# Kernel tuning notes

Hardware: AMD Instinct MI355X
Metric: run time of the kernel (lower is better)

Reference implementation:

```python
import jax, jax.numpy as jnp
import numpy as np
import math

B, DIM, N, H, G, NK = 256, 384, 128, 4, 2, 4
DH = DIM // H   # 96 head dim
DG = DIM // G   # 192 per offset group
KS = 7          # offset depthwise kernel
DFF = 2048
OFFSET_SCALE = 4.0
EPS = 1e-5

def _ln(x, g, b):
    m = jnp.mean(x, -1, keepdims=True)
    v = jnp.mean((x - m) ** 2, -1, keepdims=True)
    return (x - m) * jax.lax.rsqrt(v + EPS) * g + b

def _mlp2(x, W1, b1, W2, b2):
    return jax.nn.relu(x @ W1 + b1) @ W2 + b2

def _forward(q_raw, kv_raw, emb_q, ln_pq_g, ln_pq_b, emb_kv, ln_pkv_g, ln_pkv_b,
             Wq1, bq1, Wq2, bq2, Wk1, bk1, Wk2, bk2, Wv1, bv1, Wv2, bv2,
             dw_w, dw_b, pw_w, ln1_g, ln1_b, ln2_g, ln2_b, Wf1, bf1, Wf2, bf2, attn_scale):
    # learned positional encodings (Embedding + LayerNorm), added on channel-first layout
    q_raw = q_raw + _ln(emb_q[:N], ln_pq_g, ln_pq_b).T[None]           # (B, DIM, N)
    kv_raw = kv_raw + _ln(emb_kv[:N], ln_pkv_g, ln_pkv_b).T[None]
    # query projection: Linear-ReLU-Linear over channel dim (dropout = identity, eval)
    q = _mlp2(q_raw.transpose(0, 2, 1), Wq1, bq1, Wq2, bq2).transpose(0, 2, 1)  # (B, DIM, N)
    # offset prediction: depthwise conv -> GELU -> 1x1 conv -> tanh * scale
    gq = q.reshape(B * G, DG, N)
    pad = (KS - 1) // 2
    off = jax.lax.conv_general_dilated(gq, dw_w, (1,), [(pad, pad)],
                                       dimension_numbers=('NCH', 'OIH', 'NCH'),
                                       feature_group_count=DG) + dw_b[None, :, None]
    off = jax.nn.gelu(off, approximate=False)
    off = jnp.einsum('bcn,kc->bkn', off, pw_w)
    off = jnp.tanh(off) * OFFSET_SCALE                                 # (B*G, NK, N)
    vgrid = jnp.arange(N, dtype=off.dtype) + off
    vg = jnp.clip(2.0 * vgrid / (N - 1) - 1.0, -1.0, 1.0)              # (B*G, NK, N)
    # 1D bilinear grid_sample, zero padding, align_corners=False
    gkv = kv_raw.reshape(B * G, DG, N)
    iy = ((vg.reshape(B * G, NK * N) + 1.0) * N - 1.0) / 2.0           # unnormalized coord
    y0 = jnp.floor(iy)
    w = (iy - y0)[:, None, :]
    y0i = y0.astype(jnp.int32)
    def samp(yi):
        valid = ((yi >= 0) & (yi < N)).astype(gkv.dtype)[:, None, :]
        idx = jnp.broadcast_to(jnp.clip(yi, 0, N - 1)[:, None, :], (B * G, DG, NK * N))
        return jnp.take_along_axis(gkv, idx, axis=2) * valid
    sampled = samp(y0i) * (1.0 - w) + samp(y0i + 1) * w                # (B*G, DG, NK*N)
    # '(b g) num_k d n -> (b num_k) (g d) n'
    kv_feats = sampled.reshape(B, G, DG, NK, N).transpose(0, 3, 1, 2, 4).reshape(B * NK, DIM, N)
    k = _mlp2(kv_feats.transpose(0, 2, 1), Wk1, bk1, Wk2, bk2)         # (B*NK, N, DIM)
    v = _mlp2(kv_feats.transpose(0, 2, 1), Wv1, bv1, Wv2, bv2)
    # per-position attention: each query attends over its NK sampled kv
    qh = (q * DH ** -0.5).reshape(B, H, DH, N).transpose(0, 3, 1, 2)   # (B, N, H, DH)
    def heads(t):  # (B*NK, N, DIM) -> (B, N, H, NK, DH)
        return t.reshape(B, NK, N, H, DH).transpose(0, 2, 3, 1, 4)
    kh, vh = heads(k), heads(v)
    # NB: original code's `headdim = q.size(-1)` picks up the seq dim (N), kept faithfully
    sim = jnp.einsum('bnhd,bnhjd->bnhj', qh, kh) / math.sqrt(N)
    sim = sim - jax.lax.stop_gradient(jnp.max(sim, -1, keepdims=True))
    attn = jax.nn.softmax(sim * attn_scale, axis=-1)
    out = jnp.einsum('bnhj,bnhjd->bnhd', attn, vh).reshape(B, N, DIM)
    res = _ln(q_raw.transpose(0, 2, 1) + out, ln1_g, ln1_b)
    res = res + _mlp2(res, Wf1, bf1, Wf2, bf2)
    return _ln(res, ln2_g, ln2_b).transpose(0, 2, 1)                   # (B, DIM, N)

def setup_inputs() -> dict:
    key = jax.random.key(0)
    ks = iter(jax.random.split(key, 24))
    def nrm(shape, s=0.05):
        return jax.random.normal(next(ks), shape, dtype=jnp.float32) * s
    return dict(
        q_raw=jax.random.normal(next(ks), (B, DIM, N), dtype=jnp.float32),
        kv_raw=jax.random.normal(next(ks), (B, DIM, N), dtype=jnp.float32),
        emb_q=nrm((128, DIM), 1.0), ln_pq_g=jnp.ones((DIM,), jnp.float32), ln_pq_b=jnp.zeros((DIM,), jnp.float32),
        emb_kv=nrm((128, DIM), 1.0), ln_pkv_g=jnp.ones((DIM,), jnp.float32), ln_pkv_b=jnp.zeros((DIM,), jnp.float32),
        Wq1=nrm((DIM, DIM)), bq1=jnp.zeros((DIM,), jnp.float32), Wq2=nrm((DIM, DIM)), bq2=jnp.zeros((DIM,), jnp.float32),
        Wk1=nrm((DIM, DIM)), bk1=jnp.zeros((DIM,), jnp.float32), Wk2=nrm((DIM, DIM)), bk2=jnp.zeros((DIM,), jnp.float32),
        Wv1=nrm((DIM, DIM)), bv1=jnp.zeros((DIM,), jnp.float32), Wv2=nrm((DIM, DIM)), bv2=jnp.zeros((DIM,), jnp.float32),
        dw_w=nrm((DG, 1, KS)), dw_b=jnp.zeros((DG,), jnp.float32), pw_w=nrm((NK, DG)),
        ln1_g=jnp.ones((DIM,), jnp.float32), ln1_b=jnp.zeros((DIM,), jnp.float32),
        ln2_g=jnp.ones((DIM,), jnp.float32), ln2_b=jnp.zeros((DIM,), jnp.float32),
        Wf1=nrm((DIM, DFF)), bf1=jnp.zeros((DFF,), jnp.float32), Wf2=nrm((DFF, DIM)), bf2=jnp.zeros((DIM,), jnp.float32),
        attn_scale=jnp.asarray(70.0, jnp.float32),
    )

def reference(q_raw, kv_raw, emb_q, ln_pq_g, ln_pq_b, emb_kv, ln_pkv_g, ln_pkv_b,
              Wq1, bq1, Wq2, bq2, Wk1, bk1, Wk2, bk2, Wv1, bv1, Wv2, bv2,
              dw_w, dw_b, pw_w, ln1_g, ln1_b, ln2_g, ln2_b, Wf1, bf1, Wf2, bf2, attn_scale):
    return _forward(q_raw, kv_raw, emb_q, ln_pq_g, ln_pq_b, emb_kv, ln_pkv_g, ln_pkv_b,
                    Wq1, bq1, Wq2, bq2, Wk1, bk1, Wk2, bk2, Wv1, bv1, Wv2, bv2,
                    dw_w, dw_b, pw_w, ln1_g, ln1_b, ln2_g, ln2_b, Wf1, bf1, Wf2, bf2, attn_scale)
```

## Files before the change

### kernel.cpp

```cpp
#include <hip/hip_runtime.h>
#include <hip/hip_bf16.h>
#include <cstdint>
#include <cstddef>

#define BB   256
#define DIM  384
#define NN   128
#define NH   4
#define NG   2
#define NKK  4
#define DHH  96
#define DG   192
#define KSZ  7
#define DFF  2048

typedef __attribute__((ext_vector_type(8))) short bf8_t;
typedef __attribute__((ext_vector_type(4))) float f4_t;

static __device__ __forceinline__ float geluf(float x) {
  return 0.5f * x * (1.0f + erff(x * 0.70710678118654752440f));
}
static __device__ __forceinline__ short f2bf(float f) {
  union { __hip_bfloat16 h; short s; } u;
  u.h = __float2bfloat16(f);
  return u.s;
}

template<bool WB>
__global__ __launch_bounds__(128) void ln_rows_kernel(
    const float* __restrict__ X,
    const float* __restrict__ gam, const float* __restrict__ bet,
    float* __restrict__ out, __hip_bfloat16* __restrict__ out2)
{
  const int row = blockIdx.x;
  const int t = threadIdx.x;
  const size_t base = (size_t)row * DIM;
  float x0 = X[base + t], x1 = X[base + t + 128], x2 = X[base + t + 256];
  __shared__ float ws[2];
  float s = x0 + x1 + x2;
#pragma unroll
  for (int o = 32; o; o >>= 1) s += __shfl_down(s, o);
  if ((t & 63) == 0) ws[t >> 6] = s;
  __syncthreads();
  const float m = (ws[0] + ws[1]) * (1.0f / DIM);
  __syncthreads();
  const float d0 = x0 - m, d1 = x1 - m, d2 = x2 - m;
  float v = d0 * d0 + d1 * d1 + d2 * d2;
#pragma unroll
  for (int o = 32; o; o >>= 1) v += __shfl_down(v, o);
  if ((t & 63) == 0) ws[t >> 6] = v;
  __syncthreads();
  const float var = (ws[0] + ws[1]) * (1.0f / DIM);
  const float rs = rsqrtf(var + 1e-5f);
  const float o0 = d0 * rs * gam[t]       + bet[t];
  const float o1 = d1 * rs * gam[t + 128] + bet[t + 128];
  const float o2 = d2 * rs * gam[t + 256] + bet[t + 256];
  out[base + t] = o0; out[base + t + 128] = o1; out[base + t + 256] = o2;
  if (WB) {
    out2[base + t]       = __float2bfloat16(o0);
    out2[base + t + 128] = __float2bfloat16(o1);
    out2[base + t + 256] = __float2bfloat16(o2);
  }
}

template<bool WB>
__global__ __launch_bounds__(256) void transpose_addpe(
    const float* __restrict__ X, const float* __restrict__ pe,
    float* __restrict__ out, __hip_bfloat16* __restrict__ outb)
{
  __shared__ float tile[32][33];
  const int b = blockIdx.z;
  const int n0 = blockIdx.x * 32, d0 = blockIdx.y * 32;
  const int tx = threadIdx.x, ty = threadIdx.y;
#pragma unroll
  for (int i = 0; i < 4; i++) {
    const int d = d0 + ty + i * 8;
    tile[ty + i * 8][tx] = X[(size_t)b * DIM * NN + (size_t)d * NN + n0 + tx];
  }
  __syncthreads();
#pragma unroll
  for (int i = 0; i < 4; i++) {
    const int n = n0 + ty + i * 8;
    const int d = d0 + tx;
    const float v = tile[tx][ty + i * 8] + pe[n * DIM + d];
    out[((size_t)b * NN + n) * DIM + d] = v;
    if (WB) outb[((size_t)b * NN + n) * DIM + d] = __float2bfloat16(v);
  }
}

__global__ __launch_bounds__(256) void transpose_to_cf(
    const float* __restrict__ rows, float* __restrict__ out)
{
  __shared__ float tile[32][33];
  const int b = blockIdx.z;
  const int n0 = blockIdx.x * 32, d0 = blockIdx.y * 32;
  const int tx = threadIdx.x, ty = threadIdx.y;
#pragma unroll
  for (int i = 0; i < 4; i++) {
    const int n = n0 + ty + i * 8;
    tile[ty + i * 8][tx] = rows[((size_t)b * NN + n) * DIM + d0 + tx];
  }
  __syncthreads();
#pragma unroll
  for (int i = 0; i < 4; i++) {
    const int d = d0 + ty + i * 8;
    out[(size_t)b * DIM * NN + (size_t)d * NN + n0 + tx] = tile[tx][ty + i * 8];
  }
}

__global__ __launch_bounds__(256) void wtrans_kernel(
    const float* __restrict__ W, __hip_bfloat16* __restrict__ WT, int K, int N)
{
  __shared__ float tile[32][33];
  const int n0 = blockIdx.x * 32, k0 = blockIdx.y * 32;
  const int tx = threadIdx.x, ty = threadIdx.y;
#pragma unroll
  for (int i = 0; i < 4; i++)
    tile[ty + i * 8][tx] = W[(size_t)(k0 + ty + i * 8) * N + n0 + tx];
  __syncthreads();
#pragma unroll
  for (int i = 0; i < 4; i++)
    WT[(size_t)(n0 + ty + i * 8) * K + k0 + tx] =
        __float2bfloat16(tile[tx][ty + i * 8]);
}

#define LDP 40
template<bool RELU, bool RES, bool OUTBF>
__global__ __launch_bounds__(256) void mfma_gemm_kernel(
    const __hip_bfloat16* __restrict__ A, const __hip_bfloat16* __restrict__ BT,
    const float* __restrict__ bias, const float* __restrict__ resid,
    float* __restrict__ outf, __hip_bfloat16* __restrict__ outb,
    int K, int Nc, int lda)
{
  __shared__ __align__(16) short As[128 * LDP];
  __shared__ __align__(16) short Bs[128 * LDP];
  const int tid = threadIdx.x;
  const int lane = tid & 63, wid = tid >> 6;
  const int wm = wid >> 1, wn = wid & 1;
  const size_t rowBase = (size_t)blockIdx.y * 128;
  const size_t colBase = (size_t)blockIdx.x * 128;
  f4_t acc[4][4] = {};
  const int lr = lane & 15, lg = lane >> 4;
  for (int k0 = 0; k0 < K; k0 += 32) {
#pragma unroll
    for (int l = 0; l < 2; l++) {
      const int c = tid + l * 256;
      const int r = c >> 2, ko = (c & 3) * 8;
      *(uint4*)&As[r * LDP + ko] =
          *(const uint4*)&A[(rowBase + r) * (size_t)lda + k0 + ko];
      *(uint4*)&Bs[r * LDP + ko] =
          *(const uint4*)&BT[(colBase + r) * (size_t)K + k0 + ko];
    }
    __syncthreads();
    bf8_t af[4], bfr[4];
#pragma unroll
    for (int mi = 0; mi < 4; mi++)
      af[mi] = *(const bf8_t*)&As[(wm * 64 + mi * 16 + lr) * LDP + lg * 8];
#pragma unroll
    for (int ni = 0; ni < 4; ni++)
      bfr[ni] = *(const bf8_t*)&Bs[(wn * 64 + ni * 16 + lr) * LDP + lg * 8];
#pragma unroll
    for (int mi = 0; mi < 4; mi++)
#pragma unroll
      for (int ni = 0; ni < 4; ni++)
        acc[mi][ni] = __builtin_amdgcn_mfma_f32_16x16x32_bf16(
            af[mi], bfr[ni], acc[mi][ni], 0, 0, 0);
    __syncthreads();
  }
#pragma unroll
  for (int ni = 0; ni < 4; ni++) {
    const size_t col = colBase + wn * 64 + ni * 16 + lr;
    const float bv = bias[col];
#pragma unroll
    for (int mi = 0; mi < 4; mi++) {
#pragma unroll
      for (int r = 0; r < 4; r++) {
        const size_t row = rowBase + wm * 64 + mi * 16 + lg * 4 + r;
        float v = acc[mi][ni][r] + bv;
        if (RELU) v = fmaxf(v, 0.0f);
        if (RES) v += resid[row * Nc + col];
        if (OUTBF) outb[row * Nc + col] = __float2bfloat16(v);
        else       outf[row * Nc + col] = v;
      }
    }
  }
}

__global__ __launch_bounds__(256) void mfma_gemm_sampled_kv(
    const float* __restrict__ kvrows, const int* __restrict__ y0buf,
    const float* __restrict__ wbuf, const __hip_bfloat16* __restrict__ BT,
    const float* __restrict__ biasK, const float* __restrict__ biasV,
    __hip_bfloat16* __restrict__ outb, int byBase)
{
  const int K = DIM, Nc = 2 * DIM;
  __shared__ __align__(16) short As[128 * LDP];
  __shared__ __align__(16) short Bs[128 * LDP];
  const int tid = threadIdx.x;
  const int lane = tid & 63, wid = tid >> 6;
  const int wm = wid >> 1, wn = wid & 1;
  const int byG = blockIdx.y + byBase;
  const int b = byG >> 2, kk = byG & 3;
  const size_t rowBase = (size_t)blockIdx.y * 128;
  const size_t colBase = (size_t)blockIdx.x * 128;
  f4_t acc[4][4] = {};
  const int lr = lane & 15, lg = lane >> 4;
  for (int k0 = 0; k0 < K; k0 += 32) {
#pragma unroll
    for (int l = 0; l < 2; l++) {
      const int c = tid + l * 256;
      const int r = c >> 2, ko = (c & 3) * 8;
      const int d = k0 + ko;
      const int g = d / DG;
      const int sidx = (((b * NG + g) * NKK) + kk) * NN + r;
      const int y0 = y0buf[sidx];
      const float w = wbuf[sidx];
      float4 a0 = make_float4(0.f, 0.f, 0.f, 0.f), a1 = a0, b0 = a0, b1 = a0;
      if (y0 >= 0) {
        const float* p = &kvrows[((size_t)b * NN + y0) * DIM + d];
        a0 = *(const float4*)p; a1 = *(const float4*)(p + 4);
      }
      if (y0 < NN - 1) {
        const float* p = &kvrows[((size_t)b * NN + y0 + 1) * DIM + d];
        b0 = *(const float4*)p; b1 = *(const float4*)(p + 4);
      }
      const float w0 = 1.0f - w;
      short sv[8];
      sv[0] = f2bf(a0.x * w0 + b0.x * w); sv[1] = f2bf(a0.y * w0 + b0.y * w);
      sv[2] = f2bf(a0.z * w0 + b0.z * w); sv[3] = f2bf(a0.w * w0 + b0.w * w);
      sv[4] = f2bf(a1.x * w0 + b1.x * w); sv[5] = f2bf(a1.y * w0 + b1.y * w);
      sv[6] = f2bf(a1.z * w0 + b1.z * w); sv[7] = f2bf(a1.w * w0 + b1.w * w);
      *(uint4*)&As[r * LDP + ko] = *(const uint4*)&sv[0];
      *(uint4*)&Bs[r * LDP + ko] =
          *(const uint4*)&BT[(colBase + r) * (size_t)K + k0 + ko];
    }
    __syncthreads();
    bf8_t af[4], bfr[4];
#pragma unroll
    for (int mi = 0; mi < 4; mi++)
      af[mi] = *(const bf8_t*)&As[(wm * 64 + mi * 16 + lr) * LDP + lg * 8];
#pragma unroll
    for (int ni = 0; ni < 4; ni++)
      bfr[ni] = *(const bf8_t*)&Bs[(wn * 64 + ni * 16 + lr) * LDP + lg * 8];
#pragma unroll
    for (int mi = 0; mi < 4; mi++)
#pragma unroll
      for (int ni = 0; ni < 4; ni++)
        acc[mi][ni] = __builtin_amdgcn_mfma_f32_16x16x32_bf16(
            af[mi], bfr[ni], acc[mi][ni], 0, 0, 0);
    __syncthreads();
  }
  const float* bp = (colBase < (size_t)DIM) ? biasK : biasV;
  const int cofs = (colBase < (size_t)DIM) ? 0 : DIM;
#pragma unroll
  for (int ni = 0; ni < 4; ni++) {
    const size_t col = colBase + wn * 64 + ni * 16 + lr;
    const float bv = bp[col - cofs];
#pragma unroll
    for (int mi = 0; mi < 4; mi++) {
#pragma unroll
      for (int r = 0; r < 4; r++) {
        const size_t row = rowBase + wm * 64 + mi * 16 + lg * 4 + r;
        const float v = fmaxf(acc[mi][ni][r] + bv, 0.0f);
        outb[row * Nc + col] = __float2bfloat16(v);
      }
    }
  }
}

__global__ __launch_bounds__(192) void offset3_kernel(
    const float* __restrict__ qproj, const float* __restrict__ dw_w,
    const float* __restrict__ dw_b, const float* __restrict__ pw_w,
    int* __restrict__ y0buf, float* __restrict__ wbuf)
{
  const int bg = blockIdx.x;
  const int n0 = blockIdx.y * 16;
  const int b = bg >> 1, g = bg & 1;
  const int t = threadIdx.x;
  const int lane = t & 63, wv = t >> 6;
  __shared__ float part[16][3][4];

  const float* qp = qproj + (size_t)b * NN * DIM + g * DG + t;
  float dwc[KSZ];
#pragma unroll
  for (int tap = 0; tap < KSZ; ++tap) dwc[tap] = dw_w[t * KSZ + tap];
  const float db = dw_b[t];
  const float pw0 = pw_w[0 * DG + t], pw1 = pw_w[1 * DG + t];
  const float pw2 = pw_w[2 * DG + t], pw3 = pw_w[3 * DG + t];

  float x[16 + KSZ - 1];
#pragma unroll
  for (int j = 0; j < 16 + KSZ - 1; ++j) {
    const int np = n0 - 3 + j;
    x[j] = ((unsigned)np < (unsigned)NN) ? qp[(size_t)np * DIM] : 0.f;
  }
#pragma unroll
  for (int j = 0; j < 16; ++j) {
    float y = db;
#pragma unroll
    for (int i = 0; i < KSZ; ++i) y = fmaf(x[j + i], dwc[i], y);
    const float gl = geluf(y);
    float p0 = pw0 * gl, p1 = pw1 * gl, p2 = pw2 * gl, p3 = pw3 * gl;
#pragma unroll
    for (int o = 32; o; o >>= 1) {
      p0 += __shfl_down(p0, o);
      p1 += __shfl_down(p1, o);
      p2 += __shfl_down(p2, o);
      p3 += __shfl_down(p3, o);
    }
    if (lane == 0) {
      part[j][wv][0] = p0; part[j][wv][1] = p1;
      part[j][wv][2] = p2; part[j][wv][3] = p3;
    }
  }
  __syncthreads();
  if (t < 64) {
    const int j = t >> 2, kk = t & 3;
    const int n = n0 + j;
    const float acc = part[j][0][kk] + part[j][1][kk] + part[j][2][kk];
    const float off = tanhf(acc) * 4.0f;
    const float vgrid = (float)n + off;
    float vg = 2.0f * vgrid / (float)(NN - 1) - 1.0f;
    vg = fminf(fmaxf(vg, -1.0f), 1.0f);
    const float iy = ((vg + 1.0f) * (float)NN - 1.0f) * 0.5f;
    const float y0f = floorf(iy);
    const int idx = (bg * NKK + kk) * NN + n;
    y0buf[idx] = (int)y0f;
    wbuf[idx] = iy - y0f;
  }
}

__global__ __launch_bounds__(128) void attn_kernel(
    const float* __restrict__ qproj, const float* __restrict__ k_ch,
    const float* __restrict__ v_ch, const float* __restrict__ attn_scale,
    float* __restrict__ qrows, int bBase)
{
  const int bid = blockIdx.x;
  const int h = bid & 3;
  const int bnl = bid >> 2;
  const int bl = bnl >> 7;
  const int n = bnl & 127;
  const size_t bn = ((size_t)(bBase + bl)) * NN + n;
  const int t = threadIdx.x;
  const int lane = t & 63, wid = t >> 6;
  __shared__ float red[2][4];
  __shared__ float simsh[4];
  float qv = 0.f;
  if (t < DHH)
    qv = qproj[bn * DIM + h * DHH + t] * 0.10206207261596577f;
#pragma unroll
  for (int kk = 0; kk < NKK; kk++) {
    float pv = 0.f;
    if (t < DHH)
      pv = qv * k_ch[(((size_t)bl * NKK + kk) * NN + n) * DIM + h * DHH + t];
#pragma unroll
    for (int o = 32; o; o >>= 1) pv += __shfl_down(pv, o);
    if (lane == 0) red[wid][kk] = pv;
  }
  __syncthreads();
  if (t == 0) {
#pragma unroll
    for (int kk = 0; kk < NKK; kk++)
      simsh[kk] = (red[0][kk] + red[1][kk]) * 0.08838834764831845f;
  }
  __syncthreads();
  const float s0 = simsh[0], s1 = simsh[1], s2 = simsh[2], s3 = simsh[3];
  const float m = fmaxf(fmaxf(s0, s1), fmaxf(s2, s3));
  const float sc = attn_scale[0];
  const float e0 = expf((s0 - m) * sc), e1 = expf((s1 - m) * sc);
  const float e2 = expf((s2 - m) * sc), e3 = expf((s3 - m) * sc);
  const float inv = 1.0f / (e0 + e1 + e2 + e3);
  if (t < DHH) {
    const size_t vb = ((size_t)bl * NKK * NN + n) * DIM + h * DHH + t;
    const size_t stride = (size_t)NN * DIM;
    float o = e0 * inv * v_ch[vb];
    o += e1 * inv * v_ch[vb + stride];
    o += e2 * inv * v_ch[vb + 2 * stride];
    o += e3 * inv * v_ch[vb + 3 * stride];
    const size_t oi = bn * DIM + h * DHH + t;
    qrows[oi] = qrows[oi] + o;
  }
}

extern "C" void kernel_launch(void* const* d_in, const int* in_sizes, int n_in,
                              void* d_out, int out_size, void* d_ws, size_t ws_size,
                              hipStream_t stream)
{
  const float* q_raw    = (const float*)d_in[0];
  const float* kv_raw   = (const float*)d_in[1];
  const float* emb_q    = (const float*)d_in[2];
  const float* ln_pq_g  = (const float*)d_in[3];
  const float* ln_pq_b  = (const float*)d_in[4];
  const float* emb_kv   = (const float*)d_in[5];
  const float* ln_pkv_g = (const float*)d_in[6];
  const float* ln_pkv_b = (const float*)d_in[7];
  const float* Wq1 = (const float*)d_in[8];   const float* bq1 = (const float*)d_in[9];
  const float* Wq2 = (const float*)d_in[10];  const float* bq2 = (const float*)d_in[11];
  const float* Wk1 = (const float*)d_in[12];  const float* bk1 = (const float*)d_in[13];
  const float* Wk2 = (const float*)d_in[14];  const float* bk2 = (const float*)d_in[15];
  const float* Wv1 = (const float*)d_in[16];  const float* bv1 = (const float*)d_in[17];
  const float* Wv2 = (const float*)d_in[18];  const float* bv2 = (const float*)d_in[19];
  const float* dw_w = (const float*)d_in[20]; const float* dw_b = (const float*)d_in[21];
  const float* pw_w = (const float*)d_in[22];
  const float* ln1_g = (const float*)d_in[23]; const float* ln1_b = (const float*)d_in[24];
  const float* ln2_g = (const float*)d_in[25]; const float* ln2_b = (const float*)d_in[26];
  const float* Wf1 = (const float*)d_in[27];  const float* bf1 = (const float*)d_in[28];
  const float* Wf2 = (const float*)d_in[29];  const float* bf2 = (const float*)d_in[30];
  const float* attn_scale = (const float*)d_in[31];
  float* out = (float*)d_out;

  const size_t S = (size_t)BB * NN * DIM;
  const size_t TAILF = 4 * 73728 + 147456 + 2 * 393216 + 2 * (size_t)NN * DIM
                     + 2 * (size_t)BB * NG * NKK * NN;
  int NCH = 16, NFQ = 8;
  {
    const int cand[5][2] = {{2, 1}, {4, 1}, {8, 2}, {16, 4}, {16, 8}};
    for (int i = 0; i < 5; i++) {
      const size_t rows = (size_t)(BB / cand[i][0]) * NKK * NN;
      size_t ch = S;
      const size_t pb = rows * 1152;
      const size_t pc = S / 2 + (size_t)33554432 / cand[i][1];
      if (pb > ch) ch = pb;
      if (pc > ch) ch = pc;
      const size_t totB = (3 * S + ch + TAILF) * 4;
      if (totB <= ws_size) { NCH = cand[i][0]; NFQ = cand[i][1]; break; }
    }
  }
  const int MQ = BB * NN;
  const int B_PER_CH = BB / NCH;
  const int BY_PER_CH = B_PER_CH * NKK;
  const int ROWS_PER_CH = BY_PER_CH * NN;
  const int FROWS = MQ / NFQ;
  size_t CHSZ = S;
  {
    const size_t pb = (size_t)ROWS_PER_CH * 1152;
    const size_t pc = S / 2 + (size_t)33554432 / NFQ;
    if (pb > CHSZ) CHSZ = pb;
    if (pc > CHSZ) CHSZ = pc;
  }

  float* wsf = (float*)d_ws;
  float* qrows = wsf;
  float* kvr   = qrows + S;
  float* qproj = kvr + S;
  float* chbase = qproj + S;
  __hip_bfloat16* qrows_bf = (__hip_bfloat16*)chbase;
  __hip_bfloat16* scr_bf   = (__hip_bfloat16*)(chbase + S / 2);
  __hip_bfloat16* hidkv_bf = (__hip_bfloat16*)chbase;
  float* k_ch = chbase + (size_t)ROWS_PER_CH * DIM;
  float* v_ch = k_ch + (size_t)ROWS_PER_CH * DIM;
  __hip_bfloat16* res_bf = (__hip_bfloat16*)chbase;
  __hip_bfloat16* ffnh   = (__hip_bfloat16*)(chbase + S / 2);
  float* p = chbase + CHSZ;
  __hip_bfloat16* wtq1  = (__hip_bfloat16*)p; p += 73728;
  __hip_bfloat16* wtq2  = (__hip_bfloat16*)p; p += 73728;
  __hip_bfloat16* wtkv1 = (__hip_bfloat16*)p; p += 147456;
  __hip_bfloat16* wtk2  = (__hip_bfloat16*)p; p += 73728;
  __hip_bfloat16* wtv2  = (__hip_bfloat16*)p; p += 73728;
  __hip_bfloat16* wtf1  = (__hip_bfloat16*)p; p += 393216;
  __hip_bfloat16* wtf2  = (__hip_bfloat16*)p; p += 393216;
  float* peq  = p; p += (size_t)NN * DIM;
  float* pekv = p; p += (size_t)NN * DIM;
  int*   y0buf = (int*)p; p += (size_t)BB * NG * NKK * NN;
  float* wbuf  = p;
  float* res   = kvr;
  float* res2  = qproj;
  float* lnout = qrows;

  wtrans_kernel<<<dim3(DIM/32, DIM/32), dim3(32, 8), 0, stream>>>(Wq1, wtq1, DIM, DIM);
  wtrans_kernel<<<dim3(DIM/32, DIM/32), dim3(32, 8), 0, stream>>>(Wq2, wtq2, DIM, DIM);
  wtrans_kernel<<<dim3(DIM/32, DIM/32), dim3(32, 8), 0, stream>>>(Wk1, wtkv1, DIM, DIM);
  wtrans_kernel<<<dim3(DIM/32, DIM/32), dim3(32, 8), 0, stream>>>(
      Wv1, wtkv1 + (size_t)DIM * DIM, DIM, DIM);
  wtrans_kernel<<<dim3(DIM/32, DIM/32), dim3(32, 8), 0, stream>>>(Wk2, wtk2, DIM, DIM);
  wtrans_kernel<<<dim3(DIM/32, DIM/32), dim3(32, 8), 0, stream>>>(Wv2, wtv2, DIM, DIM);
  wtrans_kernel<<<dim3(DFF/32, DIM/32), dim3(32, 8), 0, stream>>>(Wf1, wtf1, DIM, DFF);
  wtrans_kernel<<<dim3(DIM/32, DFF/32), dim3(32, 8), 0, stream>>>(Wf2, wtf2, DFF, DIM);

  ln_rows_kernel<false><<<dim3(NN), dim3(128), 0, stream>>>(
      emb_q, ln_pq_g, ln_pq_b, peq, nullptr);
  ln_rows_kernel<false><<<dim3(NN), dim3(128), 0, stream>>>(
      emb_kv, ln_pkv_g, ln_pkv_b, pekv, nullptr);

  transpose_addpe<true><<<dim3(NN/32, DIM/32, BB), dim3(32, 8), 0, stream>>>(
      q_raw, peq, qrows, qrows_bf);
  transpose_addpe<false><<<dim3(NN/32, DIM/32, BB), dim3(32, 8), 0, stream>>>(
      kv_raw, pekv, kvr, nullptr);

  mfma_gemm_kernel<true, false, true><<<dim3(DIM/128, MQ/128), 256, 0, stream>>>(
      qrows_bf, wtq1, bq1, nullptr, nullptr, scr_bf, DIM, DIM, DIM);
  mfma_gemm_kernel<false, false, false><<<dim3(DIM/128, MQ/128), 256, 0, stream>>>(
      scr_bf, wtq2, bq2, nullptr, qproj, nullptr, DIM, DIM, DIM);

  offset3_kernel<<<dim3(BB * NG, NN / 16), dim3(192), 0, stream>>>(
      qproj, dw_w, dw_b, pw_w, y0buf, wbuf);

  for (int c = 0; c < NCH; ++c) {
    const int byBase = c * BY_PER_CH;
    mfma_gemm_sampled_kv<<<dim3(2 * DIM / 128, BY_PER_CH), 256, 0, stream>>>(
        kvr, y0buf, wbuf, wtkv1, bk1, bv1, hidkv_bf, byBase);
    mfma_gemm_kernel<false, false, false><<<dim3(DIM/128, ROWS_PER_CH/128), 256, 0, stream>>>(
        hidkv_bf, wtk2, bk2, nullptr, k_ch, nullptr, DIM, DIM, 2 * DIM);
    mfma_gemm_kernel<false, false, false><<<dim3(DIM/128, ROWS_PER_CH/128), 256, 0, stream>>>(
        hidkv_bf + DIM, wtv2, bv2, nullptr, v_ch, nullptr, DIM, DIM, 2 * DIM);
    attn_kernel<<<dim3(B_PER_CH * NN * NH), 128, 0, stream>>>(
        qproj, k_ch, v_ch, attn_scale, qrows, c * B_PER_CH);
  }

  ln_rows_kernel<true><<<dim3(MQ), dim3(128), 0, stream>>>(
      qrows, ln1_g, ln1_b, res, res_bf);

  for (int q = 0; q < NFQ; ++q) {
    const size_t roff = (size_t)q * FROWS;
    mfma_gemm_kernel<true, false, true><<<dim3(DFF/128, FROWS/128), 256, 0, stream>>>(
        res_bf + roff * DIM, wtf1, bf1, nullptr, nullptr, ffnh, DIM, DFF, DIM);
    mfma_gemm_kernel<false, true, false><<<dim3(DIM/128, FROWS/128), 256, 0, stream>>>(
        ffnh, wtf2, bf2, res + roff * DIM, res2 + roff * DIM, nullptr, DFF, DIM, DFF);
  }

  ln_rows_kernel<false><<<dim3(MQ), dim3(128), 0, stream>>>(
      res2, ln2_g, ln2_b, lnout, nullptr);
  transpose_to_cf<<<dim3(NN/32, DIM/32, BB), dim3(32, 8), 0, stream>>>(
      lnout, out);
}
```

Measured before the change: 1.266 ms.

## Split bilinear sampling out of KV GEMM, merge K/V second GEMMs, add XCD swizzle

```diff
diff --git a/kernel.cpp b/kernel.cpp
--- a/kernel.cpp
+++ b/kernel.cpp
@@ -26,6 +26,18 @@
   return u.s;
 }
 
+static __device__ __forceinline__ void xcd_swizzle(int& bx, int& by) {
+  const int gx = gridDim.x;
+  const int nwg = gx * gridDim.y;
+  const int flat = by * gx + bx;
+  const int q = nwg >> 3, r = nwg & 7;
+  const int xcd = flat & 7, idx = flat >> 3;
+  const int logical =
+      (xcd < r ? xcd * (q + 1) : r * (q + 1) + (xcd - r) * q) + idx;
+  bx = logical % gx;
+  by = logical / gx;
+}
+
 template<bool WB>
 __global__ __launch_bounds__(128) void ln_rows_kernel(
     const float* __restrict__ X,
@@ -124,6 +136,14 @@
         __float2bfloat16(tile[tx][ty + i * 8]);
 }
 
+__global__ __launch_bounds__(256) void concat_bias_kernel(
+    const float* __restrict__ a, const float* __restrict__ b,
+    float* __restrict__ o, int n)
+{
+  const int i = blockIdx.x * 256 + threadIdx.x;
+  if (i < 2 * n) o[i] = (i < n) ? a[i] : b[i - n];
+}
+
 #define LDP 40
 template<bool RELU, bool RES, bool OUTBF>
 __global__ __launch_bounds__(256) void mfma_gemm_kernel(
@@ -137,8 +157,10 @@
   const int tid = threadIdx.x;
   const int lane = tid & 63, wid = tid >> 6;
   const int wm = wid >> 1, wn = wid & 1;
-  const size_t rowBase = (size_t)blockIdx.y * 128;
-  const size_t colBase = (size_t)blockIdx.x * 128;
+  int bx = blockIdx.x, by = blockIdx.y;
+  xcd_swizzle(bx, by);
+  const size_t rowBase = (size_t)by * 128;
+  const size_t colBase = (size_t)bx * 128;
   f4_t acc[4][4] = {};
   const int lr = lane & 15, lg = lane >> 4;
   for (int k0 = 0; k0 < K; k0 += 32) {
@@ -186,22 +208,29 @@
   }
 }
 
-__global__ __launch_bounds__(256) void mfma_gemm_sampled_kv(
-    const float* __restrict__ kvrows, const int* __restrict__ y0buf,
-    const float* __restrict__ wbuf, const __hip_bfloat16* __restrict__ BT,
+__global__ __launch_bounds__(256) void mfma_gemm_kv2(
+    const __hip_bfloat16* __restrict__ hidkv,
+    const __hip_bfloat16* __restrict__ BTk, const __hip_bfloat16* __restrict__ BTv,
     const float* __restrict__ biasK, const float* __restrict__ biasV,
-    __hip_bfloat16* __restrict__ outb, int byBase)
-{
-  const int K = DIM, Nc = 2 * DIM;
+    float* __restrict__ outK, float* __restrict__ outV)
+{
+  const int K = DIM, Nc = DIM, lda = 2 * DIM;
   __shared__ __align__(16) short As[128 * LDP];
   __shared__ __align__(16) short Bs[128 * LDP];
   const int tid = threadIdx.x;
   const int lane = tid & 63, wid = tid >> 6;
   const int wm = wid >> 1, wn = wid & 1;
-  const int byG = blockIdx.y + byBase;
-  const int b = byG >> 2, kk = byG & 3;
-  const size_t rowBase = (size_t)blockIdx.y * 128;
-  const size_t colBase = (size_t)blockIdx.x * 128;
+  int bx = blockIdx.x, by = blockIdx.y;
+  xcd_swizzle(bx, by);
+  const int nbyh = gridDim.y >> 1;
+  const int half = (by >= nbyh) ? 1 : 0;
+  const int byl = by - half * nbyh;
+  const __hip_bfloat16* A = hidkv + half * DIM;
+  const __hip_bfloat16* BT = half ? BTv : BTk;
+  const float* bias = half ? biasV : biasK;
+  float* outf = half ? outV : outK;
+  const size_t rowBase = (size_t)byl * 128;
+  const size_t colBase = (size_t)bx * 128;
   f4_t acc[4][4] = {};
   const int lr = lane & 15, lg = lane >> 4;
   for (int k0 = 0; k0 < K; k0 += 32) {
@@ -209,27 +238,8 @@
     for (int l = 0; l < 2; l++) {
       const int c = tid + l * 256;
       const int r = c >> 2, ko = (c & 3) * 8;
-      const int d = k0 + ko;
-      const int g = d / DG;
-      const int sidx = (((b * NG + g) * NKK) + kk) * NN + r;
-      const int y0 = y0buf[sidx];
-      const float w = wbuf[sidx];
-      float4 a0 = make_float4(0.f, 0.f, 0.f, 0.f), a1 = a0, b0 = a0, b1 = a0;
-      if (y0 >= 0) {
-        const float* p = &kvrows[((size_t)b * NN + y0) * DIM + d];
-        a0 = *(const float4*)p; a1 = *(const float4*)(p + 4);
-      }
-      if (y0 < NN - 1) {
-        const float* p = &kvrows[((size_t)b * NN + y0 + 1) * DIM + d];
-        b0 = *(const float4*)p; b1 = *(const float4*)(p + 4);
-      }
-      const float w0 = 1.0f - w;
-      short sv[8];
-      sv[0] = f2bf(a0.x * w0 + b0.x * w); sv[1] = f2bf(a0.y * w0 + b0.y * w);
-      sv[2] = f2bf(a0.z * w0 + b0.z * w); sv[3] = f2bf(a0.w * w0 + b0.w * w);
-      sv[4] = f2bf(a1.x * w0 + b1.x * w); sv[5] = f2bf(a1.y * w0 + b1.y * w);
-      sv[6] = f2bf(a1.z * w0 + b1.z * w); sv[7] = f2bf(a1.w * w0 + b1.w * w);
-      *(uint4*)&As[r * LDP + ko] = *(const uint4*)&sv[0];
+      *(uint4*)&As[r * LDP + ko] =
+          *(const uint4*)&A[(rowBase + r) * (size_t)lda + k0 + ko];
       *(uint4*)&Bs[r * LDP + ko] =
           *(const uint4*)&BT[(colBase + r) * (size_t)K + k0 + ko];
     }
@@ -249,22 +259,52 @@
             af[mi], bfr[ni], acc[mi][ni], 0, 0, 0);
     __syncthreads();
   }
-  const float* bp = (colBase < (size_t)DIM) ? biasK : biasV;
-  const int cofs = (colBase < (size_t)DIM) ? 0 : DIM;
 #pragma unroll
   for (int ni = 0; ni < 4; ni++) {
     const size_t col = colBase + wn * 64 + ni * 16 + lr;
-    const float bv = bp[col - cofs];
+    const float bv = bias[col];
 #pragma unroll
     for (int mi = 0; mi < 4; mi++) {
 #pragma unroll
       for (int r = 0; r < 4; r++) {
         const size_t row = rowBase + wm * 64 + mi * 16 + lg * 4 + r;
-        const float v = fmaxf(acc[mi][ni][r] + bv, 0.0f);
-        outb[row * Nc + col] = __float2bfloat16(v);
+        outf[row * Nc + col] = acc[mi][ni][r] + bv;
       }
     }
   }
+}
+
+__global__ __launch_bounds__(256) void sample_rows_kernel(
+    const float* __restrict__ kvrows, const int* __restrict__ y0buf,
+    const float* __restrict__ wbuf, __hip_bfloat16* __restrict__ outb,
+    int byBase)
+{
+  const int gid = blockIdx.x * 256 + threadIdx.x;
+  const int rowl = gid / 48, c8 = gid - rowl * 48;
+  const int d = c8 * 8;
+  const int n = rowl & (NN - 1);
+  const int byG = byBase + (rowl >> 7);
+  const int b = byG >> 2, kk = byG & 3;
+  const int g = d / DG;
+  const int sidx = (((b * NG + g) * NKK) + kk) * NN + n;
+  const int y0 = y0buf[sidx];
+  const float w = wbuf[sidx];
+  float4 a0 = make_float4(0.f, 0.f, 0.f, 0.f), a1 = a0, b0 = a0, b1 = a0;
+  if (y0 >= 0) {
+    const float* p = &kvrows[((size_t)b * NN + y0) * DIM + d];
+    a0 = *(const float4*)p; a1 = *(const float4*)(p + 4);
+  }
+  if (y0 < NN - 1) {
+    const float* p = &kvrows[((size_t)b * NN + y0 + 1) * DIM + d];
+    b0 = *(const float4*)p; b1 = *(const float4*)(p + 4);
+  }
+  const float w0 = 1.0f - w;
+  short sv[8];
+  sv[0] = f2bf(a0.x * w0 + b0.x * w); sv[1] = f2bf(a0.y * w0 + b0.y * w);
+  sv[2] = f2bf(a0.z * w0 + b0.z * w); sv[3] = f2bf(a0.w * w0 + b0.w * w);
+  sv[4] = f2bf(a1.x * w0 + b1.x * w); sv[5] = f2bf(a1.y * w0 + b1.y * w);
+  sv[6] = f2bf(a1.z * w0 + b1.z * w); sv[7] = f2bf(a1.w * w0 + b1.w * w);
+  *(uint4*)&outb[(size_t)rowl * DIM + d] = *(const uint4*)&sv[0];
 }
 
 __global__ __launch_bounds__(192) void offset3_kernel(
@@ -409,15 +449,15 @@
   float* out = (float*)d_out;
 
   const size_t S = (size_t)BB * NN * DIM;
-  const size_t TAILF = 4 * 73728 + 147456 + 2 * 393216 + 2 * (size_t)NN * DIM
-                     + 2 * (size_t)BB * NG * NKK * NN;
+  const size_t TAILF = 2 * 73728 + 147456 + 2 * 73728 + 2 * 393216 + 768
+                     + 2 * (size_t)NN * DIM + 2 * (size_t)BB * NG * NKK * NN;
   int NCH = 16, NFQ = 8;
   {
     const int cand[5][2] = {{2, 1}, {4, 1}, {8, 2}, {16, 4}, {16, 8}};
     for (int i = 0; i < 5; i++) {
       const size_t rows = (size_t)(BB / cand[i][0]) * NKK * NN;
       size_t ch = S;
-      const size_t pb = rows * 1152;
+      const size_t pb = rows * 1344;
       const size_t pc = S / 2 + (size_t)33554432 / cand[i][1];
       if (pb > ch) ch = pb;
       if (pc > ch) ch = pc;
@@ -432,7 +472,7 @@
   const int FROWS = MQ / NFQ;
   size_t CHSZ = S;
   {
-    const size_t pb = (size_t)ROWS_PER_CH * 1152;
+    const size_t pb = (size_t)ROWS_PER_CH * 1344;
     const size_t pc = S / 2 + (size_t)33554432 / NFQ;
     if (pb > CHSZ) CHSZ = pb;
     if (pc > CHSZ) CHSZ = pc;
@@ -445,8 +485,9 @@
   float* chbase = qproj + S;
   __hip_bfloat16* qrows_bf = (__hip_bfloat16*)chbase;
   __hip_bfloat16* scr_bf   = (__hip_bfloat16*)(chbase + S / 2);
-  __hip_bfloat16* hidkv_bf = (__hip_bfloat16*)chbase;
-  float* k_ch = chbase + (size_t)ROWS_PER_CH * DIM;
+  __hip_bfloat16* sampA_bf = (__hip_bfloat16*)chbase;
+  __hip_bfloat16* hidkv_bf = (__hip_bfloat16*)(chbase + (size_t)ROWS_PER_CH * 192);
+  float* k_ch = chbase + (size_t)ROWS_PER_CH * 576;
   float* v_ch = k_ch + (size_t)ROWS_PER_CH * DIM;
   __hip_bfloat16* res_bf = (__hip_bfloat16*)chbase;
   __hip_bfloat16* ffnh   = (__hip_bfloat16*)(chbase + S / 2);
@@ -458,6 +499,7 @@
   __hip_bfloat16* wtv2  = (__hip_bfloat16*)p; p += 73728;
   __hip_bfloat16* wtf1  = (__hip_bfloat16*)p; p += 393216;
   __hip_bfloat16* wtf2  = (__hip_bfloat16*)p; p += 393216;
+  float* bkv1 = p; p += 768;
   float* peq  = p; p += (size_t)NN * DIM;
   float* pekv = p; p += (size_t)NN * DIM;
   int*   y0buf = (int*)p; p += (size_t)BB * NG * NKK * NN;
@@ -475,6 +517,7 @@
   wtrans_kernel<<<dim3(DIM/32, DIM/32), dim3(32, 8), 0, stream>>>(Wv2, wtv2, DIM, DIM);
   wtrans_kernel<<<dim3(DFF/32, DIM/32), dim3(32, 8), 0, stream>>>(Wf1, wtf1, DIM, DFF);
   wtrans_kernel<<<dim3(DIM/32, DFF/32), dim3(32, 8), 0, stream>>>(Wf2, wtf2, DFF, DIM);
+  concat_bias_kernel<<<dim3(3), dim3(256), 0, stream>>>(bk1, bv1, bkv1, DIM);
 
   ln_rows_kernel<false><<<dim3(NN), dim3(128), 0, stream>>>(
       emb_q, ln_pq_g, ln_pq_b, peq, nullptr);
@@ -496,12 +539,12 @@
 
   for (int c = 0; c < NCH; ++c) {
     const int byBase = c * BY_PER_CH;
-    mfma_gemm_sampled_kv<<<dim3(2 * DIM / 128, BY_PER_CH), 256, 0, stream>>>(
-        kvr, y0buf, wbuf, wtkv1, bk1, bv1, hidkv_bf, byBase);
-    mfma_gemm_kernel<false, false, false><<<dim3(DIM/128, ROWS_PER_CH/128), 256, 0, stream>>>(
-        hidkv_bf, wtk2, bk2, nullptr, k_ch, nullptr, DIM, DIM, 2 * DIM);
-    mfma_gemm_kernel<false, false, false><<<dim3(DIM/128, ROWS_PER_CH/128), 256, 0, stream>>>(
-        hidkv_bf + DIM, wtv2, bv2, nullptr, v_ch, nullptr, DIM, DIM, 2 * DIM);
+    sample_rows_kernel<<<dim3(ROWS_PER_CH * 3 / 16), 256, 0, stream>>>(
+        kvr, y0buf, wbuf, sampA_bf, byBase);
+    mfma_gemm_kernel<true, false, true><<<dim3(2*DIM/128, ROWS_PER_CH/128), 256, 0, stream>>>(
+        sampA_bf, wtkv1, bkv1, nullptr, nullptr, hidkv_bf, DIM, 2*DIM, DIM);
+    mfma_gemm_kv2<<<dim3(DIM/128, 2 * ROWS_PER_CH/128), 256, 0, stream>>>(
+        hidkv_bf, wtk2, wtv2, bk2, bv2, k_ch, v_ch);
     attn_kernel<<<dim3(B_PER_CH * NN * NH), 128, 0, stream>>>(
         qproj, k_ch, v_ch, attn_scale, qrows, c * B_PER_CH);
   }
```

Result: faster. 1.143 ms (-9.7%).
